# Optimization experiments

Measured on AMD Instinct MI355X. Metric: run time of the kernel, lower is better.

Reference implementation:

```python
import jax, jax.numpy as jnp
import numpy as np

G = 1024   # number of glimpses
P = 1024   # points per glimpse
N = G * P  # total points


def _pool(pos, batch, start, size):
    """voxel_mean_pool index computation: unique (batch, voxel) cells."""
    vox = np.floor((pos - start) / size).astype(np.int64)
    vox -= vox.min(axis=0)
    dims = vox.max(axis=0) + 1
    key = ((batch * dims[0] + vox[:, 0]) * dims[1] + vox[:, 1]) * dims[2] + vox[:, 2]
    uniq, first, inv = np.unique(key, return_index=True, return_inverse=True)
    return inv.astype(np.int64), batch[first].astype(np.int64), int(uniq.shape[0])


def setup_inputs() -> dict:
    rng = np.random.default_rng(0)
    pos = rng.uniform(-1.0, 1.0, (N, 3)).astype(np.float32)
    rgb = rng.random((N, 1)).astype(np.float32)
    batch = np.repeat(np.arange(G, dtype=np.int64), P)
    # min_pos gets a random negative offset (noise) in the torch code
    min_pos = pos.min(axis=0) - rng.random(3).astype(np.float32)
    # level-1 voxel pooling (size 0.25)
    cluster1, batch1, M1 = _pool(pos, batch, min_pos, 0.25)
    cnt1 = np.bincount(cluster1, minlength=M1).astype(np.float32)[:, None]
    ps1 = np.zeros((M1, 3), np.float32)
    np.add.at(ps1, cluster1, pos)
    ps1 /= cnt1
    # level-2 voxel pooling (size 0.5) on voxel centers
    cluster2, batch2, M2 = _pool(ps1, batch1, min_pos, 0.5)

    def lin(fi, fo):
        return (rng.standard_normal((fi, fo)).astype(np.float32) / np.sqrt(fi))

    d = dict(
        rgb=jnp.asarray(rgb), pos=jnp.asarray(pos),
        glimpse_center=jnp.asarray(rng.standard_normal((G, 3)).astype(np.float32)),
        W1l=jnp.asarray(lin(1 + 3, 16)), b1l=jnp.zeros(16, jnp.float32),
        W1g=jnp.asarray(lin(16, 32)), b1g=jnp.zeros(32, jnp.float32),
        W2l=jnp.asarray(lin(32 + 3, 64)), b2l=jnp.zeros(64, jnp.float32),
        W2g=jnp.asarray(lin(64, 128)), b2g=jnp.zeros(128, jnp.float32),
        W3l=jnp.asarray(lin(128 + 3, 128)), b3l=jnp.zeros(128, jnp.float32),
        W3g=jnp.asarray(lin(128, 256)), b3g=jnp.zeros(256, jnp.float32),
        Wlin=jnp.asarray(lin(256, 256)), blin=jnp.zeros(256, jnp.float32),
        eps=jnp.asarray(rng.standard_normal((G, 128)).astype(np.float32)),
        glimpse_index=jnp.asarray(batch),
        cluster1=jnp.asarray(cluster1), cluster2=jnp.asarray(cluster2),
        batch2=jnp.asarray(batch2),
        num_voxels1=M1, num_voxels2=M2,
    )
    return d


def _seg_mean(x, seg, m):
    s = jax.ops.segment_sum(x, seg, num_segments=m)
    c = jax.ops.segment_sum(jnp.ones((x.shape[0], 1), x.dtype), seg, num_segments=m)
    return s / jnp.maximum(c, 1.0)


def _point_conv(x_in, pos_in, pos_out, out_index, Wl, bl, Wg, bg, m_out):
    # gather: relative position of each input point to its output (voxel) center
    rel = pos_in - pos_out[out_index]                      # [E,3]
    msg = jax.nn.relu(jnp.concatenate([x_in, rel], 1) @ Wl + bl)  # [E,c_mid]
    agg = jax.ops.segment_max(msg, out_index, num_segments=m_out)  # [M,c_mid]
    return agg @ Wg + bg


def reference(rgb, pos, glimpse_center, W1l, b1l, W1g, b1g, W2l, b2l, W2g, b2g,
              W3l, b3l, W3g, b3g, Wlin, blin, eps, glimpse_index,
              cluster1, cluster2, batch2, num_voxels1, num_voxels2):
    M1, M2 = num_voxels1, num_voxels2
    Gn = glimpse_center.shape[0]
    # stage 1: voxel mean pool (0.25) + PointConv 1->16->32
    ps1 = _seg_mean(pos, cluster1, M1)                     # [M1,3]
    f1 = jax.nn.celu(_point_conv(rgb, pos, ps1, cluster1, W1l, b1l, W1g, b1g, M1))
    # stage 2: voxel mean pool (0.5) + PointConv 32->64->128
    ps2 = _seg_mean(ps1, cluster2, M2)                     # [M2,3]
    f2 = jax.nn.celu(_point_conv(f1, ps1, ps2, cluster2, W2l, b2l, W2g, b2g, M2))
    # stage 3: pool everything to the glimpse center (pos_out = zeros)
    pos_out = jnp.zeros_like(glimpse_center)
    f3 = jax.nn.celu(_point_conv(f2, ps2, pos_out, batch2, W3l, b3l, W3g, b3g, Gn))
    # head: Linear(256,256), split into mu/sigma, reparameterized sample
    out = f3 @ Wlin + blin                                 # [G,256]
    mu, s = jnp.split(out, 2, axis=1)
    sigma = jax.nn.softplus(s)
    z = mu + sigma * eps                                   # [G,128]
    z_what, z_mask = jnp.split(z, 2, axis=1)
    return z_what, z_mask, mu, sigma, f3
```

## Files before the change

### kernel.cpp

```cpp
#include <hip/hip_runtime.h>
#include <math.h>

#define N1CAP 736
#define N2CAP 192
#define S3 132

__device__ __forceinline__ float celu1(float x){ return x > 0.f ? x : (expf(x) - 1.f); }
__device__ __forceinline__ float softplus1(float x){ return fmaxf(x, 0.f) + log1pf(expf(-fabsf(x))); }
__device__ __forceinline__ void atomicMaxNonneg(float* p, float v){
    atomicMax((int*)p, __float_as_int(v));
}

__global__ __launch_bounds__(256) void kA(const float* __restrict__ rgb,
                                          const float* __restrict__ pos,
                                          const int* __restrict__ cl1,
                                          const float* __restrict__ W1l,
                                          const float* __restrict__ b1l,
                                          float* __restrict__ ps1,
                                          float* __restrict__ agg1,
                                          float* __restrict__ cnt1,
                                          int* __restrict__ seg1, int P){
    __shared__ float shx[N1CAP], shy[N1CAP], shz[N1CAP], shc[N1CAP];
    __shared__ float sha[N1CAP*16];
    __shared__ int red[2];
    const int g = blockIdx.x, tid = threadIdx.x;
    const int base = g * P;

    if (tid == 0){ red[0] = 0x7fffffff; red[1] = -1; }
    __syncthreads();
    int mn = 0x7fffffff, mx = -1;
    for (int i = tid; i < P; i += 256){ int c = cl1[base+i]; mn = min(mn,c); mx = max(mx,c); }
    atomicMin(&red[0], mn); atomicMax(&red[1], mx);
    __syncthreads();
    const int s1 = red[0];
    const int n1 = red[1] - red[0] + 1;
    const bool fast = (n1 <= N1CAP);

    if (fast){
        for (int l = tid; l < n1; l += 256){ shx[l]=0.f; shy[l]=0.f; shz[l]=0.f; shc[l]=0.f; }
        for (int t = tid; t < n1*16; t += 256) sha[t] = 0.f;
        __syncthreads();
        for (int i = tid; i < P; i += 256){
            int idx = base + i; int c = cl1[idx] - s1;
            atomicAdd(&shx[c], pos[3*idx+0]);
            atomicAdd(&shy[c], pos[3*idx+1]);
            atomicAdd(&shz[c], pos[3*idx+2]);
            atomicAdd(&shc[c], 1.0f);
        }
        __syncthreads();
        for (int l = tid; l < n1; l += 256){
            float ic = 1.0f / shc[l];
            shx[l] *= ic; shy[l] *= ic; shz[l] *= ic;
        }
        __syncthreads();
        for (int i = tid; i < P; i += 256){
            int idx = base + i; int c = cl1[idx] - s1;
            float in0 = rgb[idx];
            float r0 = pos[3*idx+0] - shx[c];
            float r1 = pos[3*idx+1] - shy[c];
            float r2 = pos[3*idx+2] - shz[c];
            float* dst = &sha[c*16];
            #pragma unroll
            for (int j = 0; j < 16; ++j){
                float v = b1l[j] + in0*W1l[j] + r0*W1l[16+j] + r1*W1l[32+j] + r2*W1l[48+j];
                atomicMaxNonneg(&dst[(j + c) & 15], fmaxf(v, 0.0f));
            }
        }
        __syncthreads();
        for (int t = tid; t < n1*3; t += 256){
            int l = t/3, d = t - 3*l;
            ps1[(size_t)s1*3 + t] = (d==0) ? shx[l] : ((d==1) ? shy[l] : shz[l]);
        }
        for (int t = tid; t < n1*16; t += 256){
            int l = t >> 4, j = t & 15;
            agg1[(size_t)s1*16 + t] = sha[l*16 + ((j + l) & 15)];
        }
    } else {
        for (int t = tid; t < n1;    t += 256) cnt1[s1+t] = 0.f;
        for (int t = tid; t < n1*3;  t += 256) ps1[(size_t)s1*3+t] = 0.f;
        for (int t = tid; t < n1*16; t += 256) agg1[(size_t)s1*16+t] = 0.f;
        __syncthreads();
        for (int i = tid; i < P; i += 256){
            int idx = base + i; int c = cl1[idx];
            atomicAdd(&ps1[3*c+0], pos[3*idx+0]);
            atomicAdd(&ps1[3*c+1], pos[3*idx+1]);
            atomicAdd(&ps1[3*c+2], pos[3*idx+2]);
            atomicAdd(&cnt1[c], 1.0f);
        }
        __syncthreads();
        for (int l = tid; l < n1; l += 256){
            float ic = 1.0f / cnt1[s1+l];
            ps1[(size_t)(s1+l)*3+0] *= ic; ps1[(size_t)(s1+l)*3+1] *= ic; ps1[(size_t)(s1+l)*3+2] *= ic;
        }
        __syncthreads();
        for (int i = tid; i < P; i += 256){
            int idx = base + i; int c = cl1[idx];
            float in0 = rgb[idx];
            float r0 = pos[3*idx+0] - ps1[3*c+0];
            float r1 = pos[3*idx+1] - ps1[3*c+1];
            float r2 = pos[3*idx+2] - ps1[3*c+2];
            #pragma unroll
            for (int j = 0; j < 16; ++j){
                float v = b1l[j] + in0*W1l[j] + r0*W1l[16+j] + r1*W1l[32+j] + r2*W1l[48+j];
                atomicMaxNonneg(&agg1[(size_t)c*16+j], fmaxf(v, 0.0f));
            }
        }
    }
    if (tid == 0){ seg1[2*g] = s1; seg1[2*g+1] = n1; }
}

__global__ __launch_bounds__(256) void kB(const float* __restrict__ ps1,
                                          const float* __restrict__ agg1,
                                          const int* __restrict__ cl2,
                                          const float* __restrict__ W1g,
                                          const float* __restrict__ b1g,
                                          const float* __restrict__ W2l,
                                          const float* __restrict__ b2l,
                                          const int* __restrict__ seg1,
                                          float* __restrict__ ps2,
                                          float* __restrict__ agg2,
                                          float* __restrict__ cnt2,
                                          int* __restrict__ seg2){
    __shared__ float sx[N2CAP], sy[N2CAP], sz[N2CAP], sc[N2CAP];
    __shared__ float sagg[N2CAP*64];
    __shared__ int red[2];
    const int g = blockIdx.x, tid = threadIdx.x;
    const int s1 = seg1[2*g], n1 = seg1[2*g+1], e1 = s1 + n1;

    if (tid == 0){ red[0] = 0x7fffffff; red[1] = -1; }
    __syncthreads();
    int mn = 0x7fffffff, mx = -1;
    for (int m = s1 + tid; m < e1; m += 256){ int c = cl2[m]; mn = min(mn,c); mx = max(mx,c); }
    atomicMin(&red[0], mn); atomicMax(&red[1], mx);
    __syncthreads();
    const int s2 = red[0];
    const int n2 = red[1] - red[0] + 1;
    const bool fast = (n2 <= N2CAP);

    if (fast){
        for (int l = tid; l < n2; l += 256){ sx[l]=0.f; sy[l]=0.f; sz[l]=0.f; sc[l]=0.f; }
        for (int t = tid; t < n2*64; t += 256) sagg[t] = 0.f;
        __syncthreads();
        for (int m = s1 + tid; m < e1; m += 256){
            int c = cl2[m] - s2;
            atomicAdd(&sx[c], ps1[3*m+0]);
            atomicAdd(&sy[c], ps1[3*m+1]);
            atomicAdd(&sz[c], ps1[3*m+2]);
            atomicAdd(&sc[c], 1.0f);
        }
        __syncthreads();
        for (int l = tid; l < n2; l += 256){
            float ic = 1.0f / sc[l];
            sx[l] *= ic; sy[l] *= ic; sz[l] *= ic;
        }
        __syncthreads();
        for (int t = tid; t < n2*3; t += 256){
            int l = t/3, d = t - 3*l;
            ps2[(size_t)s2*3 + t] = (d==0) ? sx[l] : ((d==1) ? sy[l] : sz[l]);
        }
        for (int m = s1 + tid; m < e1; m += 256){
            float a[16];
            const float* ar = agg1 + (size_t)m*16;
            #pragma unroll
            for (int k = 0; k < 16; ++k) a[k] = ar[k];
            float in[35];
            #pragma unroll
            for (int j = 0; j < 32; ++j){
                float v = b1g[j];
                #pragma unroll
                for (int k = 0; k < 16; ++k) v += a[k] * W1g[k*32+j];
                in[j] = celu1(v);
            }
            int c = cl2[m] - s2;
            in[32] = ps1[3*m+0] - sx[c];
            in[33] = ps1[3*m+1] - sy[c];
            in[34] = ps1[3*m+2] - sz[c];
            float* dst = &sagg[c*64];
            for (int j = 0; j < 64; ++j){
                float v = b2l[j];
                #pragma unroll
                for (int k = 0; k < 35; ++k) v += in[k] * W2l[k*64+j];
                atomicMaxNonneg(&dst[(j + c) & 63], fmaxf(v, 0.0f));
            }
        }
        __syncthreads();
        for (int t = tid; t < n2*64; t += 256){
            int l = t >> 6, j = t & 63;
            agg2[(size_t)s2*64 + t] = sagg[l*64 + ((j + l) & 63)];
        }
    } else {
        for (int t = tid; t < n2;    t += 256) cnt2[s2+t] = 0.f;
        for (int t = tid; t < n2*3;  t += 256) ps2[(size_t)s2*3+t] = 0.f;
        for (int t = tid; t < n2*64; t += 256) agg2[(size_t)s2*64+t] = 0.f;
        __syncthreads();
        for (int m = s1 + tid; m < e1; m += 256){
            int c = cl2[m];
            atomicAdd(&ps2[3*c+0], ps1[3*m+0]);
            atomicAdd(&ps2[3*c+1], ps1[3*m+1]);
            atomicAdd(&ps2[3*c+2], ps1[3*m+2]);
            atomicAdd(&cnt2[c], 1.0f);
        }
        __syncthreads();
        for (int l = tid; l < n2; l += 256){
            float ic = 1.0f / cnt2[s2+l];
            ps2[(size_t)(s2+l)*3+0] *= ic; ps2[(size_t)(s2+l)*3+1] *= ic; ps2[(size_t)(s2+l)*3+2] *= ic;
        }
        __syncthreads();
        for (int m = s1 + tid; m < e1; m += 256){
            float a[16];
            const float* ar = agg1 + (size_t)m*16;
            #pragma unroll
            for (int k = 0; k < 16; ++k) a[k] = ar[k];
            float in[35];
            #pragma unroll
            for (int j = 0; j < 32; ++j){
                float v = b1g[j];
                #pragma unroll
                for (int k = 0; k < 16; ++k) v += a[k] * W1g[k*32+j];
                in[j] = celu1(v);
            }
            int c = cl2[m];
            in[32] = ps1[3*m+0] - ps2[3*c+0];
            in[33] = ps1[3*m+1] - ps2[3*c+1];
            in[34] = ps1[3*m+2] - ps2[3*c+2];
            for (int j = 0; j < 64; ++j){
                float v = b2l[j];
                #pragma unroll
                for (int k = 0; k < 35; ++k) v += in[k] * W2l[k*64+j];
                atomicMaxNonneg(&agg2[(size_t)c*64+j], fmaxf(v, 0.0f));
            }
        }
    }
    if (tid == 0){ seg2[2*g] = s2; seg2[2*g+1] = n2; }
}

__global__ __launch_bounds__(256) void k_f2f(const float* __restrict__ agg2,
                                             const float* __restrict__ W2g,
                                             const float* __restrict__ b2g,
                                             float* __restrict__ f2, int M2){
    __shared__ float Ws[64*128];
    __shared__ float xt[32*S3];
    const int tid = threadIdx.x;
    const int m0 = blockIdx.x * 128;
    for (int t = tid; t < 64*128; t += 256) Ws[t] = W2g[t];
    const int tr = tid & 31, tc = tid >> 5;
    float acc[4][16];
    #pragma unroll
    for (int c = 0; c < 16; ++c){
        float b = b2g[tc*16 + c];
        #pragma unroll
        for (int r = 0; r < 4; ++r) acc[r][c] = b;
    }
    for (int c0 = 0; c0 < 64; c0 += 32){
        __syncthreads();
        for (int t = tid; t < 128*8; t += 256){
            int row = t >> 3, kq = t & 7;
            int m = m0 + row;
            float4 v = (m < M2) ? *(const float4*)&agg2[(size_t)m*64 + c0 + kq*4]
                                : make_float4(0.f,0.f,0.f,0.f);
            xt[(kq*4+0)*S3 + row] = v.x;
            xt[(kq*4+1)*S3 + row] = v.y;
            xt[(kq*4+2)*S3 + row] = v.z;
            xt[(kq*4+3)*S3 + row] = v.w;
        }
        __syncthreads();
        #pragma unroll 4
        for (int kk = 0; kk < 32; ++kk){
            int k = c0 + kk;
            float4 xr = *(const float4*)&xt[kk*S3 + tr*4];
            float xv[4] = {xr.x, xr.y, xr.z, xr.w};
            float wv[16];
            #pragma unroll
            for (int q = 0; q < 4; ++q){
                float4 w = *(const float4*)&Ws[k*128 + tc*16 + q*4];
                wv[q*4+0]=w.x; wv[q*4+1]=w.y; wv[q*4+2]=w.z; wv[q*4+3]=w.w;
            }
            #pragma unroll
            for (int r = 0; r < 4; ++r)
                #pragma unroll
                for (int c = 0; c < 16; ++c) acc[r][c] += xv[r]*wv[c];
        }
    }
    #pragma unroll
    for (int r = 0; r < 4; ++r){
        int m = m0 + tr*4 + r;
        if (m < M2){
            #pragma unroll
            for (int q = 0; q < 4; ++q){
                float4 o;
                o.x = celu1(acc[r][q*4+0]); o.y = celu1(acc[r][q*4+1]);
                o.z = celu1(acc[r][q*4+2]); o.w = celu1(acc[r][q*4+3]);
                *(float4*)&f2[(size_t)m*128 + tc*16 + q*4] = o;
            }
        }
    }
}

__global__ __launch_bounds__(256) void k_msg3g(const float* __restrict__ f2,
                                               const float* __restrict__ ps2,
                                               const int* __restrict__ seg2,
                                               const float* __restrict__ W3l,
                                               const float* __restrict__ b3l,
                                               float* __restrict__ agg3, int G){
    __shared__ float Wh[131*64];
    __shared__ float xt[32*S3];
    __shared__ float shAgg[128];
    const int tid = threadIdx.x;
    const int cb = blockIdx.y * 64;
    const int g0 = blockIdx.x * 2;
    const int S  = seg2[2*g0];
    const int B  = seg2[2*g0+1];
    const int n2b = (g0 + 1 < G) ? seg2[2*g0+3] : 0;
    const int T  = B + n2b;
    for (int t = tid; t < 131*64; t += 256){
        int k = t >> 6, c = t & 63;
        Wh[t] = W3l[k*128 + cb + c];
    }
    if (tid < 128) shAgg[tid] = 0.f;
    const int tr = tid & 31, tc = tid >> 5;
    float bias[8];
    #pragma unroll
    for (int c = 0; c < 8; ++c) bias[c] = b3l[cb + tc*8 + c];

    for (int w0 = 0; w0 < T; w0 += 128){
        float acc[4][8];
        #pragma unroll
        for (int r = 0; r < 4; ++r)
            #pragma unroll
            for (int c = 0; c < 8; ++c) acc[r][c] = bias[c];
        for (int c0 = 0; c0 < 128; c0 += 32){
            __syncthreads();
            for (int t = tid; t < 128*8; t += 256){
                int row = t >> 3, kq = t & 7;
                int ridx = w0 + row;
                float4 v = (ridx < T) ? *(const float4*)&f2[(size_t)(S+ridx)*128 + c0 + kq*4]
                                      : make_float4(0.f,0.f,0.f,0.f);
                xt[(kq*4+0)*S3 + row] = v.x;
                xt[(kq*4+1)*S3 + row] = v.y;
                xt[(kq*4+2)*S3 + row] = v.z;
                xt[(kq*4+3)*S3 + row] = v.w;
            }
            __syncthreads();
            #pragma unroll 8
            for (int kk = 0; kk < 32; ++kk){
                int k = c0 + kk;
                float4 xr = *(const float4*)&xt[kk*S3 + tr*4];
                float xv[4] = {xr.x, xr.y, xr.z, xr.w};
                float4 wa = *(const float4*)&Wh[k*64 + tc*8];
                float4 wb = *(const float4*)&Wh[k*64 + tc*8 + 4];
                float wv[8] = {wa.x,wa.y,wa.z,wa.w, wb.x,wb.y,wb.z,wb.w};
                #pragma unroll
                for (int r = 0; r < 4; ++r)
                    #pragma unroll
                    for (int c = 0; c < 8; ++c) acc[r][c] += xv[r]*wv[c];
            }
        }
        #pragma unroll
        for (int kk = 0; kk < 3; ++kk){
            const float* w = &Wh[(128+kk)*64 + tc*8];
            float wv[8];
            #pragma unroll
            for (int c = 0; c < 8; ++c) wv[c] = w[c];
            #pragma unroll
            for (int r = 0; r < 4; ++r){
                int ridx = w0 + tr*4 + r;
                float x = (ridx < T) ? ps2[(size_t)(S+ridx)*3 + kk] : 0.f;
                #pragma unroll
                for (int c = 0; c < 8; ++c) acc[r][c] += x*wv[c];
            }
        }
        float mx0[8], mx1[8];
        #pragma unroll
        for (int c = 0; c < 8; ++c){ mx0[c] = 0.f; mx1[c] = 0.f; }
        bool h0 = false, h1 = false;
        #pragma unroll
        for (int r = 0; r < 4; ++r){
            int ridx = w0 + tr*4 + r;
            if (ridx < T){
                bool second = (ridx >= B);
                h0 |= !second; h1 |= second;
                #pragma unroll
                for (int c = 0; c < 8; ++c){
                    float v = fmaxf(acc[r][c], 0.f);
                    mx0[c] = fmaxf(mx0[c], second ? 0.f : v);
                    mx1[c] = fmaxf(mx1[c], second ? v : 0.f);
                }
            }
        }
        if (h0){
            #pragma unroll
            for (int c = 0; c < 8; ++c) atomicMaxNonneg(&shAgg[tc*8 + c], mx0[c]);
        }
        if (h1){
            #pragma unroll
            for (int c = 0; c < 8; ++c) atomicMaxNonneg(&shAgg[64 + tc*8 + c], mx1[c]);
        }
    }
    __syncthreads();
    if (tid < 128){
        int loc = tid >> 6, c = tid & 63;
        int g = g0 + loc;
        if (loc == 0 || n2b > 0)
            agg3[(size_t)g*128 + cb + c] = shAgg[loc*64 + c];
    }
}

__global__ __launch_bounds__(256) void k_head(const float* __restrict__ agg3,
                                              const float* __restrict__ W3g,
                                              const float* __restrict__ b3g,
                                              const float* __restrict__ Wlin,
                                              const float* __restrict__ blin,
                                              const float* __restrict__ eps,
                                              float* __restrict__ out, int G){
    __shared__ float a3[128];
    __shared__ float f3s[256];
    __shared__ float hs[256];
    int g = blockIdx.x;
    int j = threadIdx.x;
    if (j < 128) a3[j] = agg3[(size_t)g*128 + j];
    __syncthreads();

    float v = b3g[j];
    for (int k = 0; k < 128; ++k) v += a3[k] * W3g[k*256 + j];
    v = celu1(v);
    f3s[j] = v;
    const size_t o_zm = (size_t)64*G, o_mu = (size_t)128*G, o_sg = (size_t)256*G, o_f3 = (size_t)384*G;
    out[o_f3 + (size_t)g*256 + j] = v;
    __syncthreads();

    float h = blin[j];
    for (int k = 0; k < 256; ++k) h += f3s[k] * Wlin[k*256 + j];
    hs[j] = h;
    __syncthreads();

    if (j < 128){
        float mu = hs[j];
        float sg = softplus1(hs[128 + j]);
        float z = mu + sg * eps[(size_t)g*128 + j];
        out[o_mu + (size_t)g*128 + j] = mu;
        out[o_sg + (size_t)g*128 + j] = sg;
        if (j < 64) out[(size_t)g*64 + j] = z;
        else        out[o_zm + (size_t)g*64 + (j - 64)] = z;
    }
}

extern "C" void kernel_launch(void* const* d_in, const int* in_sizes, int n_in,
                              void* d_out, int out_size, void* d_ws, size_t ws_size,
                              hipStream_t stream) {
    const float* rgb  = (const float*)d_in[0];
    const float* pos  = (const float*)d_in[1];
    const float* W1l  = (const float*)d_in[3];
    const float* b1l  = (const float*)d_in[4];
    const float* W1g  = (const float*)d_in[5];
    const float* b1g  = (const float*)d_in[6];
    const float* W2l  = (const float*)d_in[7];
    const float* b2l  = (const float*)d_in[8];
    const float* W2g  = (const float*)d_in[9];
    const float* b2g  = (const float*)d_in[10];
    const float* W3l  = (const float*)d_in[11];
    const float* b3l  = (const float*)d_in[12];
    const float* W3g  = (const float*)d_in[13];
    const float* b3g  = (const float*)d_in[14];
    const float* Wlin = (const float*)d_in[15];
    const float* blin = (const float*)d_in[16];
    const float* eps  = (const float*)d_in[17];
    const int* cl1 = (const int*)d_in[19];
    const int* cl2 = (const int*)d_in[20];

    const int N  = in_sizes[19];
    const int G  = in_sizes[17] / 128;
    const int M1 = in_sizes[20];
    const int M2 = in_sizes[21];
    const int P  = N / G;

    char* ws = (char*)d_ws;
    auto al = [](size_t x){ return (x + 255) & ~(size_t)255; };
    size_t off = 0;
    float* ps1  = (float*)(ws + off); off = al(off + 12ull*M1);
    size_t uni  = ((size_t)64*M1 > (size_t)512*M2) ? (size_t)64*M1 : (size_t)512*M2;
    float* agg1 = (float*)(ws + off);
    float* f2   = (float*)(ws + off);
    off = al(off + uni);
    float* cnt1 = (float*)(ws + off); off = al(off + 4ull*M1);
    float* ps2  = (float*)(ws + off); off = al(off + 12ull*M2);
    float* agg2 = (float*)(ws + off); off = al(off + 256ull*M2);
    float* cnt2 = (float*)(ws + off); off = al(off + 4ull*M2);
    float* agg3 = (float*)(ws + off); off = al(off + 512ull*G);
    int*   seg1 = (int*)  (ws + off); off = al(off + 8ull*G);
    int*   seg2 = (int*)  (ws + off); off = al(off + 8ull*G);
    if (off > ws_size) return;

    kA<<<G, 256, 0, stream>>>(rgb, pos, cl1, W1l, b1l, ps1, agg1, cnt1, seg1, P);
    kB<<<G, 256, 0, stream>>>(ps1, agg1, cl2, W1g, b1g, W2l, b2l, seg1, ps2, agg2, cnt2, seg2);
    int gx = (M2 + 127) / 128;
    k_f2f  <<<gx, 256, 0, stream>>>(agg2, W2g, b2g, f2, M2);
    dim3 g3((G + 1) / 2, 2);
    k_msg3g<<<g3, 256, 0, stream>>>(f2, ps2, seg2, W3l, b3l, agg3, G);
    k_head <<<G, 256, 0, stream>>>(agg3, W3g, b3g, Wlin, blin, eps, (float*)d_out, G);
}
```

Before: 424.0 us.

## Replace shared-memory atomics in stage-1 pooling with counting-sort per-voxel reduction

The stage-1 kernel now stages each glimpse's positions, rgb and cluster ids in shared memory. It builds a counting sort (histogram, wave prefix scan, scatter of point indices) so that one thread owns each voxel and computes its mean and 16-channel max in registers, with no float and max atomics. Stage 2 blocks its small matmuls in groups of four outputs to cut loop overhead, and the count divides are guarded against zero. The cost is more shared memory, several extra barriers, and uneven per-voxel work across threads.

```diff
diff --git a/kernel.cpp b/kernel.cpp
--- a/kernel.cpp
+++ b/kernel.cpp
@@ -20,60 +20,105 @@
                                           float* __restrict__ agg1,
                                           float* __restrict__ cnt1,
                                           int* __restrict__ seg1, int P){
-    __shared__ float shx[N1CAP], shy[N1CAP], shz[N1CAP], shc[N1CAP];
-    __shared__ float sha[N1CAP*16];
-    __shared__ int red[2];
+    __shared__ float sp[3*1024];
+    __shared__ float srgb[1024];
+    __shared__ int   ci[1024];
+    __shared__ int   cnt[N1CAP];
+    __shared__ int   start[N1CAP+1];
+    __shared__ int   cur[N1CAP];
+    __shared__ unsigned short pidx[1024];
+    __shared__ float wsh[64], bsh[16];
+    __shared__ int   red[2];
+    __shared__ int   wsum[4];
     const int g = blockIdx.x, tid = threadIdx.x;
     const int base = g * P;
+    const bool pfit = (P <= 1024);
 
     if (tid == 0){ red[0] = 0x7fffffff; red[1] = -1; }
+    if (tid < 64) wsh[tid] = W1l[tid];
+    if (tid < 16) bsh[tid] = b1l[tid];
     __syncthreads();
     int mn = 0x7fffffff, mx = -1;
-    for (int i = tid; i < P; i += 256){ int c = cl1[base+i]; mn = min(mn,c); mx = max(mx,c); }
+    for (int i = tid; i < P; i += 256){
+        int c = cl1[base+i];
+        if (pfit) ci[i] = c;
+        mn = min(mn,c); mx = max(mx,c);
+    }
     atomicMin(&red[0], mn); atomicMax(&red[1], mx);
     __syncthreads();
     const int s1 = red[0];
     const int n1 = red[1] - red[0] + 1;
-    const bool fast = (n1 <= N1CAP);
+    const bool fast = pfit && (n1 <= N1CAP);
 
     if (fast){
-        for (int l = tid; l < n1; l += 256){ shx[l]=0.f; shy[l]=0.f; shz[l]=0.f; shc[l]=0.f; }
-        for (int t = tid; t < n1*16; t += 256) sha[t] = 0.f;
+        for (int t = tid; t < 3*P; t += 256) sp[t] = pos[(size_t)base*3 + t];
+        for (int t = tid; t < P;   t += 256) srgb[t] = rgb[base + t];
+        for (int l = tid; l < n1;  l += 256) cnt[l] = 0;
+        __syncthreads();
+        for (int i = tid; i < P; i += 256) atomicAdd(&cnt[ci[i] - s1], 1);
+        __syncthreads();
+        {
+            int b3 = tid*3;
+            int a0 = (b3   < n1) ? cnt[b3]   : 0;
+            int a1 = (b3+1 < n1) ? cnt[b3+1] : 0;
+            int a2 = (b3+2 < n1) ? cnt[b3+2] : 0;
+            int s = a0+a1+a2;
+            int lane = tid & 63, wv = tid >> 6;
+            int ps = s;
+            #pragma unroll
+            for (int d = 1; d < 64; d <<= 1){
+                int t2 = __shfl_up(ps, d, 64);
+                if (lane >= d) ps += t2;
+            }
+            if (lane == 63) wsum[wv] = ps;
+            __syncthreads();
+            int woff = 0;
+            #pragma unroll
+            for (int w = 0; w < 4; ++w) woff += (w < wv) ? wsum[w] : 0;
+            int excl = woff + ps - s;
+            if (b3   < n1){ start[b3]   = excl;       cur[b3]   = excl; }
+            if (b3+1 < n1){ start[b3+1] = excl+a0;    cur[b3+1] = excl+a0; }
+            if (b3+2 < n1){ start[b3+2] = excl+a0+a1; cur[b3+2] = excl+a0+a1; }
+            if (tid == 0) start[n1] = P;
+        }
         __syncthreads();
         for (int i = tid; i < P; i += 256){
-            int idx = base + i; int c = cl1[idx] - s1;
-            atomicAdd(&shx[c], pos[3*idx+0]);
-            atomicAdd(&shy[c], pos[3*idx+1]);
-            atomicAdd(&shz[c], pos[3*idx+2]);
-            atomicAdd(&shc[c], 1.0f);
+            int slot = atomicAdd(&cur[ci[i] - s1], 1);
+            pidx[slot] = (unsigned short)i;
         }
         __syncthreads();
         for (int l = tid; l < n1; l += 256){
-            float ic = 1.0f / shc[l];
-            shx[l] *= ic; shy[l] *= ic; shz[l] *= ic;
-        }
-        __syncthreads();
-        for (int i = tid; i < P; i += 256){
-            int idx = base + i; int c = cl1[idx] - s1;
-            float in0 = rgb[idx];
-            float r0 = pos[3*idx+0] - shx[c];
-            float r1 = pos[3*idx+1] - shy[c];
-            float r2 = pos[3*idx+2] - shz[c];
-            float* dst = &sha[c*16];
-            #pragma unroll
-            for (int j = 0; j < 16; ++j){
-                float v = b1l[j] + in0*W1l[j] + r0*W1l[16+j] + r1*W1l[32+j] + r2*W1l[48+j];
-                atomicMaxNonneg(&dst[(j + c) & 15], fmaxf(v, 0.0f));
-            }
-        }
-        __syncthreads();
-        for (int t = tid; t < n1*3; t += 256){
-            int l = t/3, d = t - 3*l;
-            ps1[(size_t)s1*3 + t] = (d==0) ? shx[l] : ((d==1) ? shy[l] : shz[l]);
-        }
-        for (int t = tid; t < n1*16; t += 256){
-            int l = t >> 4, j = t & 15;
-            agg1[(size_t)s1*16 + t] = sha[l*16 + ((j + l) & 15)];
+            int s0 = start[l], e0 = start[l+1];
+            float sxv=0.f, syv=0.f, szv=0.f;
+            for (int k = s0; k < e0; ++k){
+                int i = pidx[k];
+                sxv += sp[3*i+0]; syv += sp[3*i+1]; szv += sp[3*i+2];
+            }
+            float ic = 1.0f / (float)max(e0 - s0, 1);
+            float mxp = sxv*ic, myp = syv*ic, mzp = szv*ic;
+            ps1[(size_t)(s1+l)*3+0] = mxp;
+            ps1[(size_t)(s1+l)*3+1] = myp;
+            ps1[(size_t)(s1+l)*3+2] = mzp;
+            float acc[16];
+            #pragma unroll
+            for (int j = 0; j < 16; ++j) acc[j] = 0.f;
+            for (int k = s0; k < e0; ++k){
+                int i = pidx[k];
+                float in0 = srgb[i];
+                float r0 = sp[3*i+0] - mxp;
+                float r1 = sp[3*i+1] - myp;
+                float r2 = sp[3*i+2] - mzp;
+                #pragma unroll
+                for (int j = 0; j < 16; ++j){
+                    float v = bsh[j] + in0*wsh[j] + r0*wsh[16+j] + r1*wsh[32+j] + r2*wsh[48+j];
+                    acc[j] = fmaxf(acc[j], fmaxf(v, 0.f));
+                }
+            }
+            float4* dst = (float4*)&agg1[(size_t)(s1+l)*16];
+            dst[0] = make_float4(acc[0], acc[1], acc[2], acc[3]);
+            dst[1] = make_float4(acc[4], acc[5], acc[6], acc[7]);
+            dst[2] = make_float4(acc[8], acc[9], acc[10], acc[11]);
+            dst[3] = make_float4(acc[12], acc[13], acc[14], acc[15]);
         }
     } else {
         for (int t = tid; t < n1;    t += 256) cnt1[s1+t] = 0.f;
@@ -89,7 +134,7 @@
         }
         __syncthreads();
         for (int l = tid; l < n1; l += 256){
-            float ic = 1.0f / cnt1[s1+l];
+            float ic = 1.0f / fmaxf(cnt1[s1+l], 1.0f);
             ps1[(size_t)(s1+l)*3+0] *= ic; ps1[(size_t)(s1+l)*3+1] *= ic; ps1[(size_t)(s1+l)*3+2] *= ic;
         }
         __syncthreads();
@@ -164,23 +209,33 @@
             #pragma unroll
             for (int k = 0; k < 16; ++k) a[k] = ar[k];
             float in[35];
-            #pragma unroll
-            for (int j = 0; j < 32; ++j){
-                float v = b1g[j];
-                #pragma unroll
-                for (int k = 0; k < 16; ++k) v += a[k] * W1g[k*32+j];
-                in[j] = celu1(v);
+            for (int j = 0; j < 32; j += 4){
+                float v0=b1g[j+0], v1=b1g[j+1], v2=b1g[j+2], v3=b1g[j+3];
+                #pragma unroll
+                for (int k = 0; k < 16; ++k){
+                    float x = a[k];
+                    const float* w = &W1g[k*32 + j];
+                    v0 += x*w[0]; v1 += x*w[1]; v2 += x*w[2]; v3 += x*w[3];
+                }
+                in[j+0]=celu1(v0); in[j+1]=celu1(v1); in[j+2]=celu1(v2); in[j+3]=celu1(v3);
             }
             int c = cl2[m] - s2;
             in[32] = ps1[3*m+0] - sx[c];
             in[33] = ps1[3*m+1] - sy[c];
             in[34] = ps1[3*m+2] - sz[c];
             float* dst = &sagg[c*64];
-            for (int j = 0; j < 64; ++j){
-                float v = b2l[j];
-                #pragma unroll
-                for (int k = 0; k < 35; ++k) v += in[k] * W2l[k*64+j];
-                atomicMaxNonneg(&dst[(j + c) & 63], fmaxf(v, 0.0f));
+            for (int j = 0; j < 64; j += 4){
+                float v0=b2l[j+0], v1=b2l[j+1], v2=b2l[j+2], v3=b2l[j+3];
+                #pragma unroll
+                for (int k = 0; k < 35; ++k){
+                    float x = in[k];
+                    const float* w = &W2l[k*64 + j];
+                    v0 += x*w[0]; v1 += x*w[1]; v2 += x*w[2]; v3 += x*w[3];
+                }
+                atomicMaxNonneg(&dst[(j+0 + c) & 63], fmaxf(v0, 0.0f));
+                atomicMaxNonneg(&dst[(j+1 + c) & 63], fmaxf(v1, 0.0f));
+                atomicMaxNonneg(&dst[(j+2 + c) & 63], fmaxf(v2, 0.0f));
+                atomicMaxNonneg(&dst[(j+3 + c) & 63], fmaxf(v3, 0.0f));
             }
         }
         __syncthreads();
@@ -202,7 +257,7 @@
         }
         __syncthreads();
         for (int l = tid; l < n2; l += 256){
-            float ic = 1.0f / cnt2[s2+l];
+            float ic = 1.0f / fmaxf(cnt2[s2+l], 1.0f);
             ps2[(size_t)(s2+l)*3+0] *= ic; ps2[(size_t)(s2+l)*3+1] *= ic; ps2[(size_t)(s2+l)*3+2] *= ic;
         }
         __syncthreads();
```

After: 397.5 us. 6.2% less time.
